# Kernel optimization log

Measured on AMD Instinct MI355X. Metric: run time of the kernel, lower is better.

## Reference

```python
import jax, jax.numpy as jnp
import numpy as np

N, E, IN_DIM, HID = 50000, 1600000, 128, 64
NEG_SLOPE = 0.2  # PyG GATConv default negative_slope


def _gat_layer(x, src, dst, W, a_src, a_dst, b, heads, ch, n):
    # x: [n, f_in]; W: [f_in, heads*ch]; a_src/a_dst: [heads, ch]; b: [heads*ch]
    h = (x @ W).reshape(n, heads, ch)                 # [n, H, C]
    alpha_s = jnp.sum(h * a_src, axis=-1)             # [n, H]
    alpha_d = jnp.sum(h * a_dst, axis=-1)             # [n, H]
    e = jax.nn.leaky_relu(alpha_s[src] + alpha_d[dst], NEG_SLOPE)  # [E, H]
    # segment softmax over incoming edges of each dst node
    m = jax.ops.segment_max(e, dst, num_segments=n)   # [n, H]
    ex = jnp.exp(e - m[dst])
    denom = jax.ops.segment_sum(ex, dst, num_segments=n)
    alpha = ex / (denom[dst] + 1e-16)                 # [E, H]
    # scatter-add weighted source features
    out = jax.ops.segment_sum(h[src] * alpha[:, :, None], dst, num_segments=n)  # [n, H, C]
    return out.reshape(n, heads * ch) + b


def setup_inputs() -> dict:
    key = jax.random.key(0)
    ks = jax.random.split(key, 10)
    x = jax.random.normal(ks[0], (N, IN_DIM), dtype=jnp.float32)
    edge_index = jax.random.randint(ks[1], (2, E), 0, N, dtype=jnp.int32)
    s1 = 1.0 / np.sqrt(IN_DIM).astype(np.float32)
    W1 = jax.random.uniform(ks[2], (IN_DIM, 2 * HID), jnp.float32, -s1, s1)
    a_src1 = jax.random.uniform(ks[3], (2, HID), jnp.float32, -s1, s1)
    a_dst1 = jax.random.uniform(ks[4], (2, HID), jnp.float32, -s1, s1)
    b1 = jnp.zeros((2 * HID,), jnp.float32)
    s2 = 1.0 / np.sqrt(2 * HID).astype(np.float32)
    W2 = jax.random.uniform(ks[5], (2 * HID, 1), jnp.float32, -s2, s2)
    a_src2 = jax.random.uniform(ks[6], (1, 1), jnp.float32, -s2, s2)
    a_dst2 = jax.random.uniform(ks[7], (1, 1), jnp.float32, -s2, s2)
    b2 = jnp.zeros((1,), jnp.float32)
    return {"x": x, "edge_index": edge_index, "W1": W1, "a_src1": a_src1,
            "a_dst1": a_dst1, "b1": b1, "W2": W2, "a_src2": a_src2,
            "a_dst2": a_dst2, "b2": b2}


def reference(x, edge_index, W1, a_src1, a_dst1, b1, W2, a_src2, a_dst2, b2):
    n = x.shape[0]
    # PyG GATConv adds self-loops by default
    loops = jnp.arange(n, dtype=edge_index.dtype)
    src = jnp.concatenate([edge_index[0], loops])
    dst = jnp.concatenate([edge_index[1], loops])
    h = _gat_layer(x, src, dst, W1, a_src1, a_dst1, b1, heads=2, ch=HID, n=n)
    h = jax.nn.relu(h)
    out = _gat_layer(h, src, dst, W2, a_src2, a_dst2, b2, heads=1, ch=1, n=n)
    return jax.nn.sigmoid(out)  # [n, 1]
```

## Files before the change

### kernel.cpp

```cpp
#include <hip/hip_runtime.h>
#include <hip/hip_bf16.h>
#include <hip/hip_fp16.h>

#define LEAKY_SLOPE 0.2f

__device__ __forceinline__ float leaky(float x) { return x > 0.f ? x : LEAKY_SLOPE * x; }

__device__ __forceinline__ unsigned fkey(float f)
{
    unsigned u = __float_as_uint(f);
    return (u & 0x80000000u) ? ~u : (u | 0x80000000u);
}
__device__ __forceinline__ float key_to_float(unsigned k)
{
    unsigned u = (k & 0x80000000u) ? (k & 0x7fffffffu) : ~k;
    return __uint_as_float(u);
}

__device__ __forceinline__ float bl(unsigned u) { return __uint_as_float(u << 16); }
__device__ __forceinline__ float bh(unsigned u) { return __uint_as_float(u & 0xffff0000u); }

__device__ __forceinline__ unsigned pack_bf16_pair(float lo, float hi)
{
    unsigned blv = __float_as_uint(lo);
    blv = (blv + 0x7fffu + ((blv >> 16) & 1u)) >> 16;
    unsigned bhv = __float_as_uint(hi);
    bhv = (bhv + 0x7fffu + ((bhv >> 16) & 1u)) & 0xffff0000u;
    return blv | bhv;
}

__global__ __launch_bounds__(256) void gemm1_kernel(
    const float* __restrict__ x, const float* __restrict__ W1,
    const float* __restrict__ a_s, const float* __restrict__ a_d,
    unsigned* __restrict__ h1b, float2* __restrict__ as1, float2* __restrict__ ad1,
    unsigned* __restrict__ keys, int n)
{
    __shared__ float wlds[128 * 128];
    __shared__ float smax0[8], smax1[8];
    int tid = threadIdx.x;
    for (int i = tid; i < 128 * 128; i += 256) {
        int k = i >> 7, j = i & 127;
        wlds[(k << 7) + ((j & 63) * 2 + (j >> 6))] = W1[i];
    }
    int l  = tid & 31;
    int g  = tid >> 5;
    int p0 = l * 4;
    float aS[4], aD[4];
#pragma unroll
    for (int i = 0; i < 4; ++i) {
        int p = p0 + i;
        int j = ((p & 1) << 6) + (p >> 1);
        aS[i] = a_s[j];
        aD[i] = a_d[j];
    }
    __syncthreads();
    int lane = tid & 63;
    float rmax0 = -INFINITY, rmax1 = -INFINITY;

    for (int base = blockIdx.x * 8; base < n; base += gridDim.x * 8) {
        int node = base + g;
        bool valid = node < n;
        float4 xr = make_float4(0.f, 0.f, 0.f, 0.f);
        if (valid) xr = *(const float4*)(x + (size_t)node * 128 + l * 4);
        float acc0 = 0.f, acc1 = 0.f, acc2 = 0.f, acc3 = 0.f;
#pragma unroll 8
        for (int k4 = 0; k4 < 32; ++k4) {
            int srcl = k4 + (lane & 32);
            float x0 = __shfl(xr.x, srcl);
            float x1 = __shfl(xr.y, srcl);
            float x2 = __shfl(xr.z, srcl);
            float x3 = __shfl(xr.w, srcl);
            const float4 w0 = *(const float4*)&wlds[(k4 * 4 + 0) * 128 + p0];
            const float4 w1 = *(const float4*)&wlds[(k4 * 4 + 1) * 128 + p0];
            const float4 w2 = *(const float4*)&wlds[(k4 * 4 + 2) * 128 + p0];
            const float4 w3 = *(const float4*)&wlds[(k4 * 4 + 3) * 128 + p0];
            acc0 = fmaf(x0, w0.x, acc0); acc1 = fmaf(x0, w0.y, acc1);
            acc2 = fmaf(x0, w0.z, acc2); acc3 = fmaf(x0, w0.w, acc3);
            acc0 = fmaf(x1, w1.x, acc0); acc1 = fmaf(x1, w1.y, acc1);
            acc2 = fmaf(x1, w1.z, acc2); acc3 = fmaf(x1, w1.w, acc3);
            acc0 = fmaf(x2, w2.x, acc0); acc1 = fmaf(x2, w2.y, acc1);
            acc2 = fmaf(x2, w2.z, acc2); acc3 = fmaf(x2, w2.w, acc3);
            acc0 = fmaf(x3, w3.x, acc0); acc1 = fmaf(x3, w3.y, acc1);
            acc2 = fmaf(x3, w3.z, acc2); acc3 = fmaf(x3, w3.w, acc3);
        }
        if (valid) {
            unsigned u0 = pack_bf16_pair(acc0, acc1);
            unsigned u1 = pack_bf16_pair(acc2, acc3);
            *(uint2*)&h1b[(size_t)node * 64 + 2 * l] = make_uint2(u0, u1);
            float vs0 = acc0 * aS[0] + acc2 * aS[2];
            float vs1 = acc1 * aS[1] + acc3 * aS[3];
            float vd0 = acc0 * aD[0] + acc2 * aD[2];
            float vd1 = acc1 * aD[1] + acc3 * aD[3];
#pragma unroll
            for (int off = 1; off < 32; off <<= 1) {
                vs0 += __shfl_xor(vs0, off);
                vs1 += __shfl_xor(vs1, off);
                vd0 += __shfl_xor(vd0, off);
                vd1 += __shfl_xor(vd1, off);
            }
            if (l == 0) {
                as1[node] = make_float2(vs0, vs1);
                ad1[node] = make_float2(vd0, vd1);
                rmax0 = fmaxf(rmax0, vs0);
                rmax1 = fmaxf(rmax1, vs1);
            }
        }
    }
    if (l == 0) { smax0[g] = rmax0; smax1[g] = rmax1; }
    __syncthreads();
    if (tid == 0) {
        float m0 = smax0[0], m1 = smax1[0];
#pragma unroll
        for (int i = 1; i < 8; ++i) { m0 = fmaxf(m0, smax0[i]); m1 = fmaxf(m1, smax1[i]); }
        atomicMax(&keys[0], fkey(m0));
        atomicMax(&keys[1], fkey(m1));
    }
}

#define CHUNK 8192

__global__ __launch_bounds__(256) void chist_kernel(
    const int* __restrict__ dst, int E, int NB, int NC, int* __restrict__ osc)
{
    __shared__ int h[256];
    int tid = threadIdx.x, c = blockIdx.x;
    h[tid] = 0;
    __syncthreads();
    int e0 = c * CHUNK, e1 = min(e0 + CHUNK, E);
    for (int e = e0 + tid; e < e1; e += 256)
        atomicAdd(&h[dst[e] >> 8], 1);
    __syncthreads();
    if (tid < NB) osc[tid * NC + c] = h[tid];
}

__global__ __launch_bounds__(1024) void oscan_kernel(int* __restrict__ osc, int len)
{
    __shared__ int wsum[16];
    int tid = threadIdx.x;
    int seg = (len + 1023) / 1024;
    int st = tid * seg, en = min(st + seg, len);
    int s = 0;
    for (int i = st; i < en; ++i) s += osc[i];
    int lane = tid & 63, w = tid >> 6;
    int incl = s;
#pragma unroll
    for (int off = 1; off < 64; off <<= 1) {
        int t = __shfl_up(incl, off);
        if (lane >= off) incl += t;
    }
    if (lane == 63) wsum[w] = incl;
    __syncthreads();
    int wb = 0;
    for (int i = 0; i < w; ++i) wb += wsum[i];
    int run = wb + incl - s;
    for (int i = st; i < en; ++i) { int v = osc[i]; osc[i] = run; run += v; }
}

__global__ __launch_bounds__(256) void cscatter_kernel(
    const int* __restrict__ src, const int* __restrict__ dst,
    int E, int NB, int NC, const int* __restrict__ osc, int2* __restrict__ pairs)
{
    __shared__ int cur[256];
    int tid = threadIdx.x, c = blockIdx.x;
    if (tid < NB) cur[tid] = osc[tid * NC + c];
    __syncthreads();
    int e0 = c * CHUNK, e1 = min(e0 + CHUNK, E);
    for (int e = e0 + tid; e < e1; e += 256) {
        int d = dst[e];
        int p = atomicAdd(&cur[d >> 8], 1);
        pairs[p] = make_int2(src[e], d);
    }
}

__global__ __launch_bounds__(256) void fsort_kernel(
    const int2* __restrict__ pairs, const int* __restrict__ osc,
    int E, int n, int NB, int NC,
    int* __restrict__ row_start, int* __restrict__ csr_src)
{
    __shared__ int fh[256];
    __shared__ int cur[256];
    __shared__ int wsum[4];
    int tid = threadIdx.x, b = blockIdx.x;
    int rbase = osc[b * NC];
    int rend  = (b + 1 < NB) ? osc[(b + 1) * NC] : E;
    fh[tid] = 0;
    __syncthreads();
    for (int i = rbase + tid; i < rend; i += 256)
        atomicAdd(&fh[pairs[i].y & 255], 1);
    __syncthreads();
    int v = fh[tid];
    int lane = tid & 63, w = tid >> 6;
    int incl = v;
#pragma unroll
    for (int off = 1; off < 64; off <<= 1) {
        int t = __shfl_up(incl, off);
        if (lane >= off) incl += t;
    }
    if (lane == 63) wsum[w] = incl;
    __syncthreads();
    int wb = 0;
    for (int i = 0; i < w; ++i) wb += wsum[i];
    int excl = wb + incl - v;
    int node = b * 256 + tid;
    if (node < n) row_start[node] = rbase + excl;
    cur[tid] = rbase + excl;
    __syncthreads();
    for (int i = rbase + tid; i < rend; i += 256) {
        int2 pr = pairs[i];
        int p = atomicAdd(&cur[pr.y & 255], 1);
        csr_src[p] = pr.x;
    }
    if (b == 0 && tid == 0) row_start[n] = E;
}

__global__ __launch_bounds__(256) void gather1_kernel(
    const unsigned* __restrict__ h1b, const float2* __restrict__ as1, const float2* __restrict__ ad1,
    const int* __restrict__ row_start, const int* __restrict__ csr_src,
    const float* __restrict__ b1, const float* __restrict__ W2,
    const unsigned* __restrict__ keys, float* __restrict__ h2, int n)
{
    int wid = threadIdx.x >> 6, lane = threadIdx.x & 63;
    int v = blockIdx.x * 4 + wid;
    if (v >= n) return;
    int grp = lane >> 4, li = lane & 15;

    float gm0 = key_to_float(keys[0]);
    float gm1 = key_to_float(keys[1]);

    float2 ad = ad1[v];
    float2 asv = as1[v];
    float m0 = leaky(gm0 + ad.x), m1 = leaky(gm1 + ad.y);
    float ps0 = __expf(leaky(asv.x + ad.x) - m0);
    float ps1 = __expf(leaky(asv.y + ad.y) - m1);

    float a0x = 0.f, a0y = 0.f, a0z = 0.f, a0w = 0.f;
    float a1x = 0.f, a1y = 0.f, a1z = 0.f, a1w = 0.f;
    if (grp == 0) {
        uint4 hu = *(const uint4*)&h1b[(size_t)v * 64 + li * 4];
        a0x = ps0 * bl(hu.x); a1x = ps1 * bh(hu.x);
        a0y = ps0 * bl(hu.y); a1y = ps1 * bh(hu.y);
        a0z = ps0 * bl(hu.z); a1z = ps1 * bh(hu.z);
        a0w = ps0 * bl(hu.w); a1w = ps1 * bh(hu.w);
    }
    float s0l = 0.f, s1l = 0.f;

    int t0 = row_start[v], t1 = row_start[v + 1];
    for (int t = t0; t < t1; t += 64) {
        int nv = t1 - t; if (nv > 64) nv = 64;
        int srcn = v;
        float p0 = 0.f, p1 = 0.f;
        if (lane < nv) {
            srcn = csr_src[t + lane];
            float2 as = as1[srcn];
            p0 = __expf(leaky(as.x + ad.x) - m0);
            p1 = __expf(leaky(as.y + ad.y) - m1);
        }
        s0l += p0; s1l += p1;
        int pk = (int)__builtin_bit_cast(unsigned, __floats2half2_rn(p0, p1));
        int jmax = (nv + 3) >> 2;
        for (int j = 0; j < jmax; ++j) {
            int idx = 4 * j + grp;
            int sj = __shfl(srcn, idx);
            __half2 hp = __builtin_bit_cast(__half2, (unsigned)__shfl(pk, idx));
            float w0 = __half2float(__low2half(hp));
            float w1 = __half2float(__high2half(hp));
            uint4 hu = *(const uint4*)&h1b[(size_t)sj * 64 + li * 4];
            a0x = fmaf(w0, bl(hu.x), a0x); a1x = fmaf(w1, bh(hu.x), a1x);
            a0y = fmaf(w0, bl(hu.y), a0y); a1y = fmaf(w1, bh(hu.y), a1y);
            a0z = fmaf(w0, bl(hu.z), a0z); a1z = fmaf(w1, bh(hu.z), a1z);
            a0w = fmaf(w0, bl(hu.w), a0w); a1w = fmaf(w1, bh(hu.w), a1w);
        }
    }
#pragma unroll
    for (int off = 32; off >= 1; off >>= 1) {
        s0l += __shfl_xor(s0l, off);
        s1l += __shfl_xor(s1l, off);
    }
    float inv0 = 1.f / (s0l + ps0 + 1e-16f);
    float inv1 = 1.f / (s1l + ps1 + 1e-16f);
#pragma unroll
    for (int off = 16; off <= 32; off <<= 1) {
        a0x += __shfl_xor(a0x, off); a1x += __shfl_xor(a1x, off);
        a0y += __shfl_xor(a0y, off); a1y += __shfl_xor(a1y, off);
        a0z += __shfl_xor(a0z, off); a1z += __shfl_xor(a1z, off);
        a0w += __shfl_xor(a0w, off); a1w += __shfl_xor(a1w, off);
    }
    const float4 b0v = *(const float4*)&b1[4 * li];
    const float4 b1v = *(const float4*)&b1[64 + 4 * li];
    const float4 w0v = *(const float4*)&W2[4 * li];
    const float4 w1v = *(const float4*)&W2[64 + 4 * li];
    float o;
    float hv = 0.f;
    o = fmaxf(fmaf(a0x, inv0, b0v.x), 0.f); hv = fmaf(o, w0v.x, hv);
    o = fmaxf(fmaf(a0y, inv0, b0v.y), 0.f); hv = fmaf(o, w0v.y, hv);
    o = fmaxf(fmaf(a0z, inv0, b0v.z), 0.f); hv = fmaf(o, w0v.z, hv);
    o = fmaxf(fmaf(a0w, inv0, b0v.w), 0.f); hv = fmaf(o, w0v.w, hv);
    o = fmaxf(fmaf(a1x, inv1, b1v.x), 0.f); hv = fmaf(o, w1v.x, hv);
    o = fmaxf(fmaf(a1y, inv1, b1v.y), 0.f); hv = fmaf(o, w1v.y, hv);
    o = fmaxf(fmaf(a1z, inv1, b1v.z), 0.f); hv = fmaf(o, w1v.z, hv);
    o = fmaxf(fmaf(a1w, inv1, b1v.w), 0.f); hv = fmaf(o, w1v.w, hv);
#pragma unroll
    for (int off = 1; off <= 8; off <<= 1) hv += __shfl_xor(hv, off);
    if (lane == 0) h2[v] = hv;
}

__global__ void gather2_kernel(
    const float* __restrict__ h2, const int* __restrict__ row_start, const int* __restrict__ csr_src,
    const float* __restrict__ aS2, const float* __restrict__ aD2, const float* __restrict__ b2,
    float* __restrict__ out, int n)
{
    int v = blockIdx.x * 256 + threadIdx.x;
    if (v >= n) return;
    float as2 = aS2[0], ad2c = aD2[0];
    float hv = h2[v];
    float ad = hv * ad2c;
    float e = leaky(fmaf(hv, as2, ad));
    float m = e, s = 1.f, num = hv;
    int t1 = row_start[v + 1];
    for (int t = row_start[v]; t < t1; ++t) {
        float hsv = h2[csr_src[t]];
        float en = leaky(fmaf(hsv, as2, ad));
        if (en > m) { float c = __expf(m - en); s *= c; num *= c; m = en; }
        float p = __expf(en - m);
        s += p;
        num = fmaf(p, hsv, num);
    }
    float o = num / (s + 1e-16f) + b2[0];
    out[v] = 1.f / (1.f + __expf(-o));
}

extern "C" void kernel_launch(void* const* d_in, const int* in_sizes, int n_in,
                              void* d_out, int out_size, void* d_ws, size_t ws_size,
                              hipStream_t stream)
{
    const float* x      = (const float*)d_in[0];
    const int*   eidx   = (const int*)  d_in[1];
    const float* W1     = (const float*)d_in[2];
    const float* a_src1 = (const float*)d_in[3];
    const float* a_dst1 = (const float*)d_in[4];
    const float* b1     = (const float*)d_in[5];
    const float* W2     = (const float*)d_in[6];
    const float* a_src2 = (const float*)d_in[7];
    const float* a_dst2 = (const float*)d_in[8];
    const float* b2     = (const float*)d_in[9];

    int n = in_sizes[0] / 128;
    int E = in_sizes[1] / 2;
    const int* src = eidx;
    const int* dst = eidx + E;

    int NC = (E + CHUNK - 1) / CHUNK;
    int NB = (n + 255) / 256;

    char* ws = (char*)d_ws;
    size_t off = 0;
    auto alloc = [&](size_t bytes) { size_t o = off; off += (bytes + 255) & ~(size_t)255; return o; };

    unsigned* h1b   = (unsigned*)(ws + alloc((size_t)n * 64 * 4));
    float2* as1     = (float2*)(ws + alloc((size_t)n * 8));
    float2* ad1     = (float2*)(ws + alloc((size_t)n * 8));
    float*  h2      = (float*) (ws + alloc((size_t)n * 4));
    int*    rowst   = (int*)   (ws + alloc((size_t)(n + 1) * 4));
    unsigned* keys  = (unsigned*)(ws + alloc(256));
    int*    osc     = (int*)   (ws + alloc((size_t)NB * NC * 4));
    int2*   pairs   = (int2*)  (ws + alloc((size_t)E * 8));
    int*    csr_src = (int*)   (ws + alloc((size_t)E * 4));
    (void)ws_size; (void)n_in; (void)out_size;

    hipMemsetAsync(keys, 0x00, 8, stream);

    gemm1_kernel<<<1024, 256, 0, stream>>>(x, W1, a_src1, a_dst1, h1b, as1, ad1, keys, n);

    chist_kernel<<<NC, 256, 0, stream>>>(dst, E, NB, NC, osc);
    oscan_kernel<<<1, 1024, 0, stream>>>(osc, NB * NC);
    cscatter_kernel<<<NC, 256, 0, stream>>>(src, dst, E, NB, NC, osc, pairs);
    fsort_kernel<<<NB, 256, 0, stream>>>(pairs, osc, E, n, NB, NC, rowst, csr_src);

    gather1_kernel<<<(n + 3) / 4, 256, 0, stream>>>(h1b, as1, ad1, rowst, csr_src, b1, W2,
                                                    keys, h2, n);
    gather2_kernel<<<(n + 255) / 256, 256, 0, stream>>>(h2, rowst, csr_src, a_src2, a_dst2, b2,
                                                        (float*)d_out, n);
}
```

Measured before the change: 346.6 us.

## Split layer-1 GEMM into MFMA bf16 kernel and folded attention-logit kernel

Replaces the scalar FP32 layer-1 GEMM with a bf16 MFMA kernel that stages swizzled x and W1 tiles in LDS. The attention logits are computed separately: W1 is first folded with a_src/a_dst into a 128x4 matrix, then each node's logits come from one dot product of x against it in FP32. The goal is to cut the GEMM's ALU cost, at the price of one extra read of x, two more launches, and each block reloading and converting all of W1.

```diff
diff --git a/kernel.cpp b/kernel.cpp
--- a/kernel.cpp
+++ b/kernel.cpp
@@ -3,6 +3,9 @@
 #include <hip/hip_fp16.h>
 
 #define LEAKY_SLOPE 0.2f
+
+typedef __attribute__((ext_vector_type(8))) short bf16x8;
+typedef __attribute__((ext_vector_type(4))) float f32x4;
 
 __device__ __forceinline__ float leaky(float x) { return x > 0.f ? x : LEAKY_SLOPE * x; }
 
@@ -29,91 +32,131 @@
     return blv | bhv;
 }
 
-__global__ __launch_bounds__(256) void gemm1_kernel(
-    const float* __restrict__ x, const float* __restrict__ W1,
-    const float* __restrict__ a_s, const float* __restrict__ a_d,
-    unsigned* __restrict__ h1b, float2* __restrict__ as1, float2* __restrict__ ad1,
+__global__ __launch_bounds__(256) void wtilde_kernel(
+    const float* __restrict__ W1, const float* __restrict__ a_s, const float* __restrict__ a_d,
+    float* __restrict__ wt)
+{
+    int w = threadIdx.x >> 6, l = threadIdx.x & 63;
+    float as_l = a_s[l], as_h = a_s[64 + l];
+    float ad_l = a_d[l], ad_h = a_d[64 + l];
+    for (int i = 0; i < 16; ++i) {
+        int k = blockIdx.x * 64 + w * 16 + i;
+        const float* wr = W1 + (size_t)k * 128;
+        float w_lo = wr[l], w_hi = wr[64 + l];
+        float s0 = w_lo * as_l, s1 = w_hi * as_h;
+        float d0 = w_lo * ad_l, d1 = w_hi * ad_h;
+#pragma unroll
+        for (int off = 32; off >= 1; off >>= 1) {
+            s0 += __shfl_xor(s0, off);
+            s1 += __shfl_xor(s1, off);
+            d0 += __shfl_xor(d0, off);
+            d1 += __shfl_xor(d1, off);
+        }
+        if (l == 0) *(float4*)&wt[k * 4] = make_float4(s0, s1, d0, d1);
+    }
+}
+
+__global__ __launch_bounds__(256) void alpha_kernel(
+    const float* __restrict__ x, const float* __restrict__ wt,
+    float2* __restrict__ as1, float2* __restrict__ ad1,
     unsigned* __restrict__ keys, int n)
 {
-    __shared__ float wlds[128 * 128];
-    __shared__ float smax0[8], smax1[8];
+    __shared__ float wtl[512];
+    __shared__ float m0s[4], m1s[4];
     int tid = threadIdx.x;
-    for (int i = tid; i < 128 * 128; i += 256) {
-        int k = i >> 7, j = i & 127;
-        wlds[(k << 7) + ((j & 63) * 2 + (j >> 6))] = W1[i];
-    }
-    int l  = tid & 31;
-    int g  = tid >> 5;
-    int p0 = l * 4;
-    float aS[4], aD[4];
-#pragma unroll
-    for (int i = 0; i < 4; ++i) {
-        int p = p0 + i;
-        int j = ((p & 1) << 6) + (p >> 1);
-        aS[i] = a_s[j];
-        aD[i] = a_d[j];
-    }
-    __syncthreads();
-    int lane = tid & 63;
-    float rmax0 = -INFINITY, rmax1 = -INFINITY;
-
-    for (int base = blockIdx.x * 8; base < n; base += gridDim.x * 8) {
-        int node = base + g;
-        bool valid = node < n;
-        float4 xr = make_float4(0.f, 0.f, 0.f, 0.f);
-        if (valid) xr = *(const float4*)(x + (size_t)node * 128 + l * 4);
-        float acc0 = 0.f, acc1 = 0.f, acc2 = 0.f, acc3 = 0.f;
-#pragma unroll 8
-        for (int k4 = 0; k4 < 32; ++k4) {
-            int srcl = k4 + (lane & 32);
-            float x0 = __shfl(xr.x, srcl);
-            float x1 = __shfl(xr.y, srcl);
-            float x2 = __shfl(xr.z, srcl);
-            float x3 = __shfl(xr.w, srcl);
-            const float4 w0 = *(const float4*)&wlds[(k4 * 4 + 0) * 128 + p0];
-            const float4 w1 = *(const float4*)&wlds[(k4 * 4 + 1) * 128 + p0];
-            const float4 w2 = *(const float4*)&wlds[(k4 * 4 + 2) * 128 + p0];
-            const float4 w3 = *(const float4*)&wlds[(k4 * 4 + 3) * 128 + p0];
-            acc0 = fmaf(x0, w0.x, acc0); acc1 = fmaf(x0, w0.y, acc1);
-            acc2 = fmaf(x0, w0.z, acc2); acc3 = fmaf(x0, w0.w, acc3);
-            acc0 = fmaf(x1, w1.x, acc0); acc1 = fmaf(x1, w1.y, acc1);
-            acc2 = fmaf(x1, w1.z, acc2); acc3 = fmaf(x1, w1.w, acc3);
-            acc0 = fmaf(x2, w2.x, acc0); acc1 = fmaf(x2, w2.y, acc1);
-            acc2 = fmaf(x2, w2.z, acc2); acc3 = fmaf(x2, w2.w, acc3);
-            acc0 = fmaf(x3, w3.x, acc0); acc1 = fmaf(x3, w3.y, acc1);
-            acc2 = fmaf(x3, w3.z, acc2); acc3 = fmaf(x3, w3.w, acc3);
-        }
-        if (valid) {
-            unsigned u0 = pack_bf16_pair(acc0, acc1);
-            unsigned u1 = pack_bf16_pair(acc2, acc3);
-            *(uint2*)&h1b[(size_t)node * 64 + 2 * l] = make_uint2(u0, u1);
-            float vs0 = acc0 * aS[0] + acc2 * aS[2];
-            float vs1 = acc1 * aS[1] + acc3 * aS[3];
-            float vd0 = acc0 * aD[0] + acc2 * aD[2];
-            float vd1 = acc1 * aD[1] + acc3 * aD[3];
-#pragma unroll
-            for (int off = 1; off < 32; off <<= 1) {
-                vs0 += __shfl_xor(vs0, off);
-                vs1 += __shfl_xor(vs1, off);
-                vd0 += __shfl_xor(vd0, off);
-                vd1 += __shfl_xor(vd1, off);
-            }
-            if (l == 0) {
-                as1[node] = make_float2(vs0, vs1);
-                ad1[node] = make_float2(vd0, vd1);
-                rmax0 = fmaxf(rmax0, vs0);
-                rmax1 = fmaxf(rmax1, vs1);
-            }
-        }
-    }
-    if (l == 0) { smax0[g] = rmax0; smax1[g] = rmax1; }
+    for (int i = tid; i < 512; i += 256) wtl[i] = wt[i];
+    __syncthreads();
+    int w = tid >> 6, l = tid & 63;
+    const float4 wa = *(const float4*)&wtl[l * 4];
+    const float4 wb = *(const float4*)&wtl[(64 + l) * 4];
+    float rm0 = -INFINITY, rm1 = -INFINITY;
+    for (int v = blockIdx.x * 4 + w; v < n; v += gridDim.x * 4) {
+        const float* xr = x + (size_t)v * 128;
+        float xa = xr[l], xb2 = xr[64 + l];
+        float s0 = fmaf(xa, wa.x, xb2 * wb.x);
+        float s1 = fmaf(xa, wa.y, xb2 * wb.y);
+        float d0 = fmaf(xa, wa.z, xb2 * wb.z);
+        float d1 = fmaf(xa, wa.w, xb2 * wb.w);
+#pragma unroll
+        for (int off = 32; off >= 1; off >>= 1) {
+            s0 += __shfl_xor(s0, off);
+            s1 += __shfl_xor(s1, off);
+            d0 += __shfl_xor(d0, off);
+            d1 += __shfl_xor(d1, off);
+        }
+        if (l == 0) {
+            as1[v] = make_float2(s0, s1);
+            ad1[v] = make_float2(d0, d1);
+            rm0 = fmaxf(rm0, s0);
+            rm1 = fmaxf(rm1, s1);
+        }
+    }
+    if (l == 0) { m0s[w] = rm0; m1s[w] = rm1; }
     __syncthreads();
     if (tid == 0) {
-        float m0 = smax0[0], m1 = smax1[0];
-#pragma unroll
-        for (int i = 1; i < 8; ++i) { m0 = fmaxf(m0, smax0[i]); m1 = fmaxf(m1, smax1[i]); }
+        float m0 = fmaxf(fmaxf(m0s[0], m0s[1]), fmaxf(m0s[2], m0s[3]));
+        float m1 = fmaxf(fmaxf(m1s[0], m1s[1]), fmaxf(m1s[2], m1s[3]));
         atomicMax(&keys[0], fkey(m0));
         atomicMax(&keys[1], fkey(m1));
+    }
+}
+
+__global__ __launch_bounds__(256) void gemm_mfma_kernel(
+    const float* __restrict__ x, const float* __restrict__ W1,
+    unsigned* __restrict__ h1b, int n)
+{
+    __shared__ unsigned short wl[128 * 128];
+    __shared__ unsigned short xl[64 * 128];
+    int tid = threadIdx.x;
+    int base = blockIdx.x * 64;
+
+    for (int f = tid; f < 8192; f += 256) {
+        int j = f & 127, k = (f >> 7) * 2;
+        float w0 = W1[(size_t)k * 128 + j];
+        float w1 = W1[(size_t)(k + 1) * 128 + j];
+        *(unsigned*)&wl[j * 128 + (k ^ ((j & 7) << 3))] = pack_bf16_pair(w0, w1);
+    }
+    for (int f = tid; f < 4096; f += 256) {
+        int row = f >> 6, k = (f & 63) * 2;
+        int node = base + row;
+        float2 xv = make_float2(0.f, 0.f);
+        if (node < n) xv = *(const float2*)&x[(size_t)node * 128 + k];
+        *(unsigned*)&xl[row * 128 + (k ^ ((row & 7) << 3))] = pack_bf16_pair(xv.x, xv.y);
+    }
+    __syncthreads();
+
+    int w = tid >> 6, l = tid & 63;
+    int ar = w * 16 + (l & 15);
+    int kq = (l >> 4) * 8;
+
+    bf16x8 A[4];
+#pragma unroll
+    for (int kk = 0; kk < 4; ++kk)
+        A[kk] = *(const bf16x8*)&xl[ar * 128 + ((kk * 32 + kq) ^ ((ar & 7) << 3))];
+
+    f32x4 acc[8];
+#pragma unroll
+    for (int t = 0; t < 8; ++t) acc[t] = (f32x4){0.f, 0.f, 0.f, 0.f};
+
+#pragma unroll
+    for (int t = 0; t < 8; ++t) {
+        int br = t * 16 + (l & 15);
+#pragma unroll
+        for (int kk = 0; kk < 4; ++kk) {
+            bf16x8 B = *(const bf16x8*)&wl[br * 128 + ((kk * 32 + kq) ^ ((br & 7) << 3))];
+            acc[t] = __builtin_amdgcn_mfma_f32_16x16x32_bf16(A[kk], B, acc[t], 0, 0, 0);
+        }
+    }
+
+#pragma unroll
+    for (int r = 0; r < 4; ++r) {
+        int nd = base + w * 16 + (l >> 4) * 4 + r;
+        if (nd < n) {
+#pragma unroll
+            for (int t = 0; t < 4; ++t)
+                h1b[(size_t)nd * 64 + (l & 15) + 16 * t] =
+                    pack_bf16_pair(acc[t][r], acc[t + 4][r]);
+        }
     }
 }
 
@@ -362,6 +405,7 @@
     float*  h2      = (float*) (ws + alloc((size_t)n * 4));
     int*    rowst   = (int*)   (ws + alloc((size_t)(n + 1) * 4));
     unsigned* keys  = (unsigned*)(ws + alloc(256));
+    float*  wt      = (float*) (ws + alloc(512 * 4));
     int*    osc     = (int*)   (ws + alloc((size_t)NB * NC * 4));
     int2*   pairs   = (int2*)  (ws + alloc((size_t)E * 8));
     int*    csr_src = (int*)   (ws + alloc((size_t)E * 4));
@@ -369,7 +413,9 @@
 
     hipMemsetAsync(keys, 0x00, 8, stream);
 
-    gemm1_kernel<<<1024, 256, 0, stream>>>(x, W1, a_src1, a_dst1, h1b, as1, ad1, keys, n);
+    wtilde_kernel<<<2, 256, 0, stream>>>(W1, a_src1, a_dst1, wt);
+    alpha_kernel<<<1024, 256, 0, stream>>>(x, wt, as1, ad1, keys, n);
+    gemm_mfma_kernel<<<(n + 63) / 64, 256, 0, stream>>>(x, W1, h1b, n);
 
     chist_kernel<<<NC, 256, 0, stream>>>(dst, E, NB, NC, osc);
     oscan_kernel<<<1, 1024, 0, stream>>>(osc, NB * NC);
```

Measured after the change: 341.3 us. Within noise of the previous version (-1.5%).
